# Performance work log

Measured on AMD Instinct MI355X. Metric: run time of the kernel, lower is better.

## Reference

```python
import jax, jax.numpy as jnp
import numpy as np

NUM_HEADS = 16


def _window_for_epoch(epoch: int) -> int:
    # Faithful reproduction of the module's (buggy) branch structure:
    # epoch<5 sets mask_4, elif epoch<10 sets mask_6, but then an
    # independent `if epoch < 15` overwrites with mask_8, else mask_10.
    if epoch < 15:
        return 16  # mask_8 -> w=16
    return 20      # mask_10 -> w=20


def setup_inputs() -> dict:
    key = jax.random.key(0)
    ks = jax.random.split(key, 4)
    B, N, C = 2, 2048, 1024
    x = jax.random.normal(ks[0], (B, N, C), dtype=jnp.float32)
    qkv_w = jax.random.normal(ks[1], (3 * C, C), dtype=jnp.float32) * (C ** -0.5)
    proj_w = jax.random.normal(ks[2], (C, C), dtype=jnp.float32) * (C ** -0.5)
    proj_b = jnp.zeros((C,), dtype=jnp.float32)
    return {"x": x, "qkv_w": qkv_w, "proj_w": proj_w, "proj_b": proj_b, "epoch": 0}


def reference(x, qkv_w, proj_w, proj_b, epoch):
    B, N, C = x.shape
    H = NUM_HEADS
    Dh = C // H
    scale = float(Dh // H)  # head_dim // num_heads (integer division), =4

    qkv = jnp.einsum('bnc,dc->bnd', x, qkv_w)           # [B,N,3C]
    qkv = qkv.reshape(B, N, 3, H, Dh).transpose(2, 0, 3, 1, 4)
    q, k, v = qkv[0], qkv[1], qkv[2]                    # each [B,H,N,Dh]

    attn = jnp.einsum('bhnd,bhmd->bhnm', q, k) * scale  # [B,H,N,N]

    w = _window_for_epoch(int(epoch))
    idx = jnp.arange(N)
    band = jnp.abs(idx[:, None] - idx[None, :]) <= w    # [N,N] sliding window
    # Original fills masked logits with 1e-9 (NOT -inf) before softmax.
    attn = jnp.where(band[None, None], attn, jnp.float32(1e-9))
    attn = jax.nn.softmax(attn, axis=-1)

    out = jnp.einsum('bhnm,bhmd->bhnd', attn, v)        # [B,H,N,Dh]
    out = out.transpose(0, 2, 1, 3).reshape(B, N, C)
    out = jnp.einsum('bnc,dc->bnd', out, proj_w) + proj_b
    return out
```

## Files before the change

### kernel.cpp

```cpp
#include <hip/hip_runtime.h>
#include <cstddef>


typedef _Float16 f16x8 __attribute__((ext_vector_type(8)));
typedef float    f32x4 __attribute__((ext_vector_type(4)));

#define MFMA16(a, b, c) __builtin_amdgcn_mfma_f32_16x16x32_f16((a), (b), (c), 0, 0, 0)

__device__ __forceinline__ void gl_lds16(const void* g, void* l) {
    __builtin_amdgcn_global_load_lds(
        (const __attribute__((address_space(1))) void*)g,
        (__attribute__((address_space(3))) void*)l, 16, 0, 0);
}

__device__ __forceinline__ ushort f2h(float f) {
    _Float16 h = (_Float16)f;
    return *(ushort*)&h;
}

__global__ void split_all(const float* __restrict__ x,
                          const float* __restrict__ qkvw,
                          const float* __restrict__ projw,
                          ushort* __restrict__ x16,
                          ushort* __restrict__ w16,
                          ushort* __restrict__ pw16)
{
    const int i = blockIdx.x * 256 + threadIdx.x;
    const float* src; ushort* dst; int j;
    if (i < 1048576)      { src = x;     dst = x16;  j = i; }
    else if (i < 1835008) { src = qkvw;  dst = w16;  j = i - 1048576; }
    else                  { src = projw; dst = pw16; j = i - 1835008; }

    float4 v = ((const float4*)src)[j];
    ((ushort4*)dst)[j] = make_ushort4(f2h(v.x), f2h(v.y), f2h(v.z), f2h(v.w));
}

__global__ __launch_bounds__(256, 3) void gemm_mfma(
    const ushort* __restrict__ A_g, const ushort* __restrict__ W_g,
    ushort* __restrict__ out16, int K)
{
    __shared__ ushort smem[16384];
    ushort* AS0 = smem;
    ushort* AS1 = smem + 4096;
    ushort* WS0 = smem + 8192;
    ushort* WS1 = smem + 12288;

    const int tid  = threadIdx.x;
    const int wid  = tid >> 6;
    const int lane = tid & 63;
    const int quad = lane >> 4;
    const int cl   = lane & 15;
    const int m0 = blockIdx.y * 128;
    const int n0 = blockIdx.x * 128;
    const int wm = (wid & 1) * 64;
    const int wn = (wid >> 1) * 64;

    const int srow = lane >> 2;
    const int scol = (lane & 3) * 8;

    const ushort* src = (wid < 2) ? A_g : W_g;
    ushort* dst = smem + wid * 4096;
    const int r0 = (wid < 2) ? m0 : n0;
    const int cofs = (wid & 1) * 32;

    f32x4 acc[4][4];
#pragma unroll
    for (int i = 0; i < 4; ++i)
#pragma unroll
        for (int j = 0; j < 4; ++j) acc[i][j] = (f32x4){0.f, 0.f, 0.f, 0.f};

    for (int k0 = 0; k0 < K; k0 += 64) {
#pragma unroll
        for (int c = 0; c < 8; ++c)
            gl_lds16(src + (size_t)(r0 + c * 16 + srow) * K + k0 + cofs + scol,
                     dst + c * 512);
        __syncthreads();

        f16x8 a0[4], w0[4];
#pragma unroll
        for (int i = 0; i < 4; ++i) {
            a0[i] = ((const f16x8*)AS0)[(wm + i * 16 + cl) * 4 + quad];
            w0[i] = ((const f16x8*)WS0)[(wn + i * 16 + cl) * 4 + quad];
        }
#pragma unroll
        for (int mi = 0; mi < 4; ++mi)
#pragma unroll
            for (int ni = 0; ni < 4; ++ni)
                acc[mi][ni] = MFMA16(a0[mi], w0[ni], acc[mi][ni]);

        f16x8 a1[4], w1[4];
#pragma unroll
        for (int i = 0; i < 4; ++i) {
            a1[i] = ((const f16x8*)AS1)[(wm + i * 16 + cl) * 4 + quad];
            w1[i] = ((const f16x8*)WS1)[(wn + i * 16 + cl) * 4 + quad];
        }
#pragma unroll
        for (int mi = 0; mi < 4; ++mi)
#pragma unroll
            for (int ni = 0; ni < 4; ++ni)
                acc[mi][ni] = MFMA16(a1[mi], w1[ni], acc[mi][ni]);
        __syncthreads();
    }

#pragma unroll
    for (int mi = 0; mi < 4; ++mi)
#pragma unroll
        for (int r = 0; r < 4; ++r) {
            const int gm = m0 + wm + mi * 16 + quad * 4 + r;
            const int b  = gm >> 11;
            const int nn = gm & 2047;
#pragma unroll
            for (int ni = 0; ni < 4; ++ni) {
                const int gn = n0 + wn + ni * 16 + cl;
                const int s  = gn >> 10;
                const int h  = (gn >> 6) & 15;
                const int dh = gn & 63;
                out16[(size_t)s * 4194304u + (((size_t)b * 16 + h) * 2048 + nn) * 64 + dh]
                    = f2h(acc[mi][ni][r]);
            }
        }
}

__global__ __launch_bounds__(256, 3) void gemm_proj(
    const ushort* __restrict__ A_g, const ushort* __restrict__ W_g,
    const float* __restrict__ bias, float* __restrict__ out)
{
    const int K = 1024, Nout = 1024;
    __shared__ ushort smem[12288];
    ushort* AS0 = smem;
    ushort* AS1 = smem + 2048;
    ushort* WS0 = smem + 4096;
    ushort* WS1 = smem + 8192;

    const int tid  = threadIdx.x;
    const int wid  = tid >> 6;
    const int lane = tid & 63;
    const int quad = lane >> 4;
    const int cl   = lane & 15;
    const int m0 = blockIdx.y * 64;
    const int n0 = blockIdx.x * 128;
    const int wm = (wid & 1) * 32;
    const int wn = (wid >> 1) * 64;

    const int srow = lane >> 2;
    const int scol = (lane & 3) * 8;

    f32x4 acc[2][4];
#pragma unroll
    for (int i = 0; i < 2; ++i)
#pragma unroll
        for (int j = 0; j < 4; ++j) acc[i][j] = (f32x4){0.f, 0.f, 0.f, 0.f};

    for (int k0 = 0; k0 < K; k0 += 64) {
#pragma unroll
        for (int c = 0; c < 6; ++c) {
            const int cid = wid * 6 + c;
            const ushort* s; ushort* d; int rr, pl;
            if (cid < 4)       { s = A_g; d = AS0 + cid * 512;        rr = m0 + cid * 16;        pl = 0; }
            else if (cid < 8)  { s = A_g; d = AS1 + (cid - 4) * 512;  rr = m0 + (cid - 4) * 16;  pl = 1; }
            else if (cid < 16) { s = W_g; d = WS0 + (cid - 8) * 512;  rr = n0 + (cid - 8) * 16;  pl = 0; }
            else               { s = W_g; d = WS1 + (cid - 16) * 512; rr = n0 + (cid - 16) * 16; pl = 1; }
            gl_lds16(s + (size_t)(rr + srow) * K + k0 + pl * 32 + scol, d);
        }
        __syncthreads();

        f16x8 a0[2], w0[4];
#pragma unroll
        for (int i = 0; i < 2; ++i)
            a0[i] = ((const f16x8*)AS0)[(wm + i * 16 + cl) * 4 + quad];
#pragma unroll
        for (int i = 0; i < 4; ++i)
            w0[i] = ((const f16x8*)WS0)[(wn + i * 16 + cl) * 4 + quad];
#pragma unroll
        for (int mi = 0; mi < 2; ++mi)
#pragma unroll
            for (int ni = 0; ni < 4; ++ni)
                acc[mi][ni] = MFMA16(a0[mi], w0[ni], acc[mi][ni]);

        f16x8 a1[2], w1[4];
#pragma unroll
        for (int i = 0; i < 2; ++i)
            a1[i] = ((const f16x8*)AS1)[(wm + i * 16 + cl) * 4 + quad];
#pragma unroll
        for (int i = 0; i < 4; ++i)
            w1[i] = ((const f16x8*)WS1)[(wn + i * 16 + cl) * 4 + quad];
#pragma unroll
        for (int mi = 0; mi < 2; ++mi)
#pragma unroll
            for (int ni = 0; ni < 4; ++ni)
                acc[mi][ni] = MFMA16(a1[mi], w1[ni], acc[mi][ni]);
        __syncthreads();
    }

    float bb[4];
#pragma unroll
    for (int ni = 0; ni < 4; ++ni) bb[ni] = bias[n0 + wn + ni * 16 + cl];
#pragma unroll
    for (int mi = 0; mi < 2; ++mi)
#pragma unroll
        for (int r = 0; r < 4; ++r) {
            const int gm = m0 + wm + mi * 16 + quad * 4 + r;
            float* rowp = out + (size_t)gm * Nout;
#pragma unroll
            for (int ni = 0; ni < 4; ++ni) {
                const int gn = n0 + wn + ni * 16 + cl;
                rowp[gn] = acc[mi][ni][r] + bb[ni];
            }
        }
}

__global__ __launch_bounds__(256) void attn_mfma(
    const ushort* __restrict__ qg, const ushort* __restrict__ kg,
    const ushort* __restrict__ vg,
    ushort* __restrict__ outp,
    const int* __restrict__ epoch_ptr)
{
    const int N = 2048;
    const int w = (epoch_ptr[0] < 15) ? 16 : 20;

    __shared__ ushort Pl[4][16][136];
    __shared__ ushort VT[64][136];
    __shared__ _Float16 SallRed[32][64];
    __shared__ float Sfin[64];

    const int tid  = threadIdx.x;
    const int wid  = tid >> 6;
    const int lane = tid & 63;
    const int quad = lane >> 4;
    const int cl   = lane & 15;

    const int bh = blockIdx.x >> 5;
    const int n0 = (blockIdx.x & 31) << 6;
    const int lo = max(0, n0 - w);
    const int wm = wid * 16;
    const int hi = min(N - 1, n0 + 63 + w);
    const int cnt = hi - lo + 1;

    for (int t = tid; t < 64 * 36; t += 256) {
        const int row = t / 36;
        const int c2  = 64 + (t - row * 36) * 2;
        *(unsigned*)&VT[row][c2] = 0u;
    }

    {
        const int ds = tid & 7;
        const int grp = tid >> 3;
        const ushort* vp = vg + ((size_t)bh * N + grp) * 64 + ds * 8;
        f16x8 vacc = (f16x8){0, 0, 0, 0, 0, 0, 0, 0};
#pragma unroll 8
        for (int it = 0; it < 64; ++it)
            vacc = vacc + *(const f16x8*)(vp + (size_t)it * 32 * 64);
        *(f16x8*)&SallRed[grp][ds * 8] = vacc;
    }
    __syncthreads();

    if (tid < 64) {
        float s = 0.f;
#pragma unroll
        for (int j = 0; j < 32; ++j) s += (float)SallRed[j][tid];
        Sfin[tid] = s;
    }

    for (int t = tid; t < 104 * 8; t += 256) {
        const int s  = t >> 3;
        const int db = (t & 7) * 8;
        if (s < cnt) {
            uint4 vv = *(const uint4*)(vg + (((size_t)bh * N) + lo + s) * 64 + db);
            VT[db + 0][s] = (ushort)(vv.x & 0xffff); VT[db + 1][s] = (ushort)(vv.x >> 16);
            VT[db + 2][s] = (ushort)(vv.y & 0xffff); VT[db + 3][s] = (ushort)(vv.y >> 16);
            VT[db + 4][s] = (ushort)(vv.z & 0xffff); VT[db + 5][s] = (ushort)(vv.z >> 16);
            VT[db + 6][s] = (ushort)(vv.w & 0xffff); VT[db + 7][s] = (ushort)(vv.w >> 16);
        }
    }

    const ushort* qp = qg + ((size_t)bh * N + n0 + wm + cl) * 64;
    const f16x8 aq0 = *(const f16x8*)(qp + quad * 8);
    const f16x8 aq1 = *(const f16x8*)(qp + 32 + quad * 8);

    f32x4 sacc[7];
#pragma unroll
    for (int ni = 0; ni < 7; ++ni) {
        int krow = lo + ni * 16 + cl;
        krow = min(krow, N - 1);
        const ushort* kp = kg + ((size_t)bh * N + krow) * 64;
        const f16x8 bk0 = *(const f16x8*)(kp + quad * 8);
        const f16x8 bk1 = *(const f16x8*)(kp + 32 + quad * 8);
        f32x4 s = (f32x4){0.f, 0.f, 0.f, 0.f};
        s = MFMA16(aq0, bk0, s);
        s = MFMA16(aq1, bk1, s);
        sacc[ni] = s;
    }

    float pm[4];
#pragma unroll
    for (int r = 0; r < 4; ++r) {
        const int n = n0 + wm + quad * 4 + r;
        const int jlo = max(0, n - w), jhi = min(N - 1, n + w);
        const int bc = jhi - jlo + 1;
        float mx = 1e-9f;
#pragma unroll
        for (int ni = 0; ni < 7; ++ni) {
            const int j = lo + ni * 16 + cl;
            const bool val = (j >= n - w) && (j <= n + w) && (j < N);
            const float sv = 4.0f * sacc[ni][r];
            if (val) mx = fmaxf(mx, sv);
        }
        mx = fmaxf(mx, __shfl_xor(mx, 1));
        mx = fmaxf(mx, __shfl_xor(mx, 2));
        mx = fmaxf(mx, __shfl_xor(mx, 4));
        mx = fmaxf(mx, __shfl_xor(mx, 8));
        const float em = __expf(1e-9f - mx);
        float e[7];
        float sum = 0.f;
#pragma unroll
        for (int ni = 0; ni < 7; ++ni) {
            const int j = lo + ni * 16 + cl;
            const bool val = (j >= n - w) && (j <= n + w) && (j < N);
            const float ev = val ? __expf(4.0f * sacc[ni][r] - mx) : 0.f;
            e[ni] = val ? (ev - em) : 0.f;
            sum += ev;
        }
        sum += __shfl_xor(sum, 1);
        sum += __shfl_xor(sum, 2);
        sum += __shfl_xor(sum, 4);
        sum += __shfl_xor(sum, 8);
        const float inv = 1.0f / ((float)(N - bc) * em + sum);
        pm[r] = em * inv;
#pragma unroll
        for (int ni = 0; ni < 7; ++ni)
            sacc[ni][r] = e[ni] * inv;
    }

#pragma unroll
    for (int ni = 0; ni < 7; ++ni)
#pragma unroll
        for (int r = 0; r < 4; ++r)
            Pl[wid][quad * 4 + r][ni * 16 + cl] = f2h(sacc[ni][r]);
    {
        const int prow = lane >> 2;
        const int pc = 112 + (lane & 3) * 4;
        *(uint2*)&Pl[wid][prow][pc] = make_uint2(0u, 0u);
    }

    __syncthreads();

    const int b = bh >> 4, h = bh & 15;
#pragma unroll
    for (int dn = 0; dn < 4; ++dn) {
        f32x4 o = (f32x4){0.f, 0.f, 0.f, 0.f};
#pragma unroll
        for (int k0 = 0; k0 < 128; k0 += 32) {
            const f16x8 a  = *(const f16x8*)&Pl[wid][cl][k0 + quad * 8];
            const f16x8 bb = *(const f16x8*)&VT[dn * 16 + cl][k0 + quad * 8];
            o = MFMA16(a, bb, o);
        }
        const int d = dn * 16 + cl;
        const float sv = Sfin[d];
#pragma unroll
        for (int r = 0; r < 4; ++r) {
            const int n = n0 + wm + quad * 4 + r;
            outp[((size_t)b * N + n) * 1024 + h * 64 + d] = f2h(o[r] + pm[r] * sv);
        }
    }
}

extern "C" void kernel_launch(void* const* d_in, const int* in_sizes, int n_in,
                              void* d_out, int out_size, void* d_ws, size_t ws_size,
                              hipStream_t stream)
{
    const float* x      = (const float*)d_in[0];
    const float* qkv_w  = (const float*)d_in[1];
    const float* proj_w = (const float*)d_in[2];
    const float* proj_b = (const float*)d_in[3];
    const int*   epoch  = (const int*)d_in[4];
    float* out = (float*)d_out;

    const size_t BHND = (size_t)2 * 16 * 2048 * 64;
    const size_t XN = 4194304, WN = 3145728;

    ushort* qkv16 = (ushort*)d_ws;
    ushort* q16   = qkv16;
    ushort* k16   = qkv16 + BHND;
    ushort* v16   = qkv16 + 2 * BHND;
    ushort* x16   = qkv16 + 3 * BHND;
    ushort* w16   = x16 + XN;
    ushort* pw16  = w16 + WN;
    ushort* ao    = x16;

    split_all<<<dim3(8192), dim3(256), 0, stream>>>(x, qkv_w, proj_w, x16, w16, pw16);

    gemm_mfma<<<dim3(24, 32), dim3(256), 0, stream>>>(x16, w16, qkv16, 1024);

    attn_mfma<<<dim3(1024), dim3(256), 0, stream>>>(q16, k16, v16, ao, epoch);

    gemm_proj<<<dim3(8, 64), dim3(256), 0, stream>>>(ao, pw16, proj_b, out);
}
```

Before: 161.3 us.

## Fuse V column sums into QKV GEMM epilogue and deepen proj GEMM K-step

The per-(batch,head) column sums of V were recomputed redundantly by every attention block, each reading the entire V sequence. They are now accumulated once in the QKV GEMM epilogue using warp shuffles and float atomics into a small zeroed workspace, and the attention kernel reads them from there. Separately, the projection GEMM now stages 128-wide K slices per iteration (doubling LDS use, launch bounds lowered to 2 blocks per CU) to halve barrier count. The atomics make the summation order nondeterministic, and a memset is added to the launch.

```diff
diff --git a/kernel.cpp b/kernel.cpp
--- a/kernel.cpp
+++ b/kernel.cpp
@@ -37,7 +37,7 @@
 
 __global__ __launch_bounds__(256, 3) void gemm_mfma(
     const ushort* __restrict__ A_g, const ushort* __restrict__ W_g,
-    ushort* __restrict__ out16, int K)
+    ushort* __restrict__ out16, float* __restrict__ sall, int K)
 {
     __shared__ ushort smem[16384];
     ushort* AS0 = smem;
@@ -119,18 +119,31 @@
                     = f2h(acc[mi][ni][r]);
             }
         }
-}
-
-__global__ __launch_bounds__(256, 3) void gemm_proj(
+
+    if (n0 >= 2048) {
+        const int b = (m0 + wm) >> 11;
+        const int h = ((n0 + wn) >> 6) & 15;
+#pragma unroll
+        for (int ni = 0; ni < 4; ++ni) {
+            float ps = 0.f;
+#pragma unroll
+            for (int mi = 0; mi < 4; ++mi)
+#pragma unroll
+                for (int r = 0; r < 4; ++r) ps += acc[mi][ni][r];
+            ps += __shfl_xor(ps, 16);
+            ps += __shfl_xor(ps, 32);
+            if (quad == 0)
+                atomicAdd(&sall[(b * 16 + h) * 64 + ni * 16 + cl], ps);
+        }
+    }
+}
+
+__global__ __launch_bounds__(256, 2) void gemm_proj(
     const ushort* __restrict__ A_g, const ushort* __restrict__ W_g,
     const float* __restrict__ bias, float* __restrict__ out)
 {
     const int K = 1024, Nout = 1024;
-    __shared__ ushort smem[12288];
-    ushort* AS0 = smem;
-    ushort* AS1 = smem + 2048;
-    ushort* WS0 = smem + 4096;
-    ushort* WS1 = smem + 8192;
+    __shared__ ushort smem[24576];
 
     const int tid  = threadIdx.x;
     const int wid  = tid >> 6;
@@ -151,44 +164,44 @@
 #pragma unroll
         for (int j = 0; j < 4; ++j) acc[i][j] = (f32x4){0.f, 0.f, 0.f, 0.f};
 
-    for (int k0 = 0; k0 < K; k0 += 64) {
-#pragma unroll
-        for (int c = 0; c < 6; ++c) {
-            const int cid = wid * 6 + c;
+    for (int k0 = 0; k0 < K; k0 += 128) {
+#pragma unroll
+        for (int c = 0; c < 12; ++c) {
+            const int cid = wid * 12 + c;
             const ushort* s; ushort* d; int rr, pl;
-            if (cid < 4)       { s = A_g; d = AS0 + cid * 512;        rr = m0 + cid * 16;        pl = 0; }
-            else if (cid < 8)  { s = A_g; d = AS1 + (cid - 4) * 512;  rr = m0 + (cid - 4) * 16;  pl = 1; }
-            else if (cid < 16) { s = W_g; d = WS0 + (cid - 8) * 512;  rr = n0 + (cid - 8) * 16;  pl = 0; }
-            else               { s = W_g; d = WS1 + (cid - 16) * 512; rr = n0 + (cid - 16) * 16; pl = 1; }
+            if (cid < 16) {
+                pl = cid >> 2;
+                const int ch = cid & 3;
+                s = A_g; rr = m0 + ch * 16;
+                d = smem + pl * 2048 + ch * 512;
+            } else {
+                const int wc = cid - 16;
+                pl = wc >> 3;
+                const int ch = wc & 7;
+                s = W_g; rr = n0 + ch * 16;
+                d = smem + 8192 + pl * 4096 + ch * 512;
+            }
             gl_lds16(s + (size_t)(rr + srow) * K + k0 + pl * 32 + scol, d);
         }
         __syncthreads();
 
-        f16x8 a0[2], w0[4];
-#pragma unroll
-        for (int i = 0; i < 2; ++i)
-            a0[i] = ((const f16x8*)AS0)[(wm + i * 16 + cl) * 4 + quad];
-#pragma unroll
-        for (int i = 0; i < 4; ++i)
-            w0[i] = ((const f16x8*)WS0)[(wn + i * 16 + cl) * 4 + quad];
-#pragma unroll
-        for (int mi = 0; mi < 2; ++mi)
-#pragma unroll
-            for (int ni = 0; ni < 4; ++ni)
-                acc[mi][ni] = MFMA16(a0[mi], w0[ni], acc[mi][ni]);
-
-        f16x8 a1[2], w1[4];
-#pragma unroll
-        for (int i = 0; i < 2; ++i)
-            a1[i] = ((const f16x8*)AS1)[(wm + i * 16 + cl) * 4 + quad];
-#pragma unroll
-        for (int i = 0; i < 4; ++i)
-            w1[i] = ((const f16x8*)WS1)[(wn + i * 16 + cl) * 4 + quad];
-#pragma unroll
-        for (int mi = 0; mi < 2; ++mi)
-#pragma unroll
-            for (int ni = 0; ni < 4; ++ni)
-                acc[mi][ni] = MFMA16(a1[mi], w1[ni], acc[mi][ni]);
+#pragma unroll
+        for (int pl = 0; pl < 4; ++pl) {
+            const ushort* ASp = smem + pl * 2048;
+            const ushort* WSp = smem + 8192 + pl * 4096;
+            f16x8 a[2], w[4];
+#pragma unroll
+            for (int i = 0; i < 2; ++i)
+                a[i] = ((const f16x8*)ASp)[(wm + i * 16 + cl) * 4 + quad];
+#pragma unroll
+            for (int i = 0; i < 4; ++i)
+                w[i] = ((const f16x8*)WSp)[(wn + i * 16 + cl) * 4 + quad];
+#pragma unroll
+            for (int mi = 0; mi < 2; ++mi)
+#pragma unroll
+                for (int ni = 0; ni < 4; ++ni)
+                    acc[mi][ni] = MFMA16(a[mi], w[ni], acc[mi][ni]);
+        }
         __syncthreads();
     }
 
@@ -212,6 +225,7 @@
 __global__ __launch_bounds__(256) void attn_mfma(
     const ushort* __restrict__ qg, const ushort* __restrict__ kg,
     const ushort* __restrict__ vg,
+    const float* __restrict__ sall,
     ushort* __restrict__ outp,
     const int* __restrict__ epoch_ptr)
 {
@@ -220,8 +234,6 @@
 
     __shared__ ushort Pl[4][16][136];
     __shared__ ushort VT[64][136];
-    __shared__ _Float16 SallRed[32][64];
-    __shared__ float Sfin[64];
 
     const int tid  = threadIdx.x;
     const int wid  = tid >> 6;
@@ -241,25 +253,7 @@
         const int c2  = 64 + (t - row * 36) * 2;
         *(unsigned*)&VT[row][c2] = 0u;
     }
-
-    {
-        const int ds = tid & 7;
-        const int grp = tid >> 3;
-        const ushort* vp = vg + ((size_t)bh * N + grp) * 64 + ds * 8;
-        f16x8 vacc = (f16x8){0, 0, 0, 0, 0, 0, 0, 0};
-#pragma unroll 8
-        for (int it = 0; it < 64; ++it)
-            vacc = vacc + *(const f16x8*)(vp + (size_t)it * 32 * 64);
-        *(f16x8*)&SallRed[grp][ds * 8] = vacc;
-    }
     __syncthreads();
-
-    if (tid < 64) {
-        float s = 0.f;
-#pragma unroll
-        for (int j = 0; j < 32; ++j) s += (float)SallRed[j][tid];
-        Sfin[tid] = s;
-    }
 
     for (int t = tid; t < 104 * 8; t += 256) {
         const int s  = t >> 3;
@@ -355,7 +349,7 @@
             o = MFMA16(a, bb, o);
         }
         const int d = dn * 16 + cl;
-        const float sv = Sfin[d];
+        const float sv = sall[bh * 64 + d];
 #pragma unroll
         for (int r = 0; r < 4; ++r) {
             const int n = n0 + wm + quad * 4 + r;
@@ -382,16 +376,19 @@
     ushort* q16   = qkv16;
     ushort* k16   = qkv16 + BHND;
     ushort* v16   = qkv16 + 2 * BHND;
-    ushort* x16   = qkv16 + 3 * BHND;
+    float*  sall  = (float*)(qkv16 + 3 * BHND);
+    ushort* x16   = (ushort*)(sall + 4096);
     ushort* w16   = x16 + XN;
     ushort* pw16  = w16 + WN;
     ushort* ao    = x16;
 
+    hipMemsetAsync(sall, 0, 2048 * sizeof(float), stream);
+
     split_all<<<dim3(8192), dim3(256), 0, stream>>>(x, qkv_w, proj_w, x16, w16, pw16);
 
-    gemm_mfma<<<dim3(24, 32), dim3(256), 0, stream>>>(x16, w16, qkv16, 1024);
-
-    attn_mfma<<<dim3(1024), dim3(256), 0, stream>>>(q16, k16, v16, ao, epoch);
+    gemm_mfma<<<dim3(24, 32), dim3(256), 0, stream>>>(x16, w16, qkv16, sall, 1024);
+
+    attn_mfma<<<dim3(1024), dim3(256), 0, stream>>>(q16, k16, v16, sall, ao, epoch);
 
     gemm_proj<<<dim3(8, 64), dim3(256), 0, stream>>>(ao, pw16, proj_b, out);
 }
```

Result: faster. 152.2 us (-5.6%).
